# Kernel tuning notes

Measured on AMD Instinct MI355X. Metric: run time of the kernel, lower is better.

## Reference

```python
import jax, jax.numpy as jnp
import numpy as np

B = 4096
N_FEATS = 2048
N_TAGS = 300
RNN_IN = 512
RNN_HID = 512
HID = 512


def setup_inputs() -> dict:
    key = jax.random.key(0)
    ks = jax.random.split(key, 16)
    sc = 0.05  # small weight init, like get_init_weights
    inp = {
        "v": jax.random.normal(ks[0], (B, N_FEATS), jnp.float32),
        "s": jax.random.normal(ks[1], (B, N_TAGS), jnp.float32),
        "decoder_input": jax.random.normal(ks[2], (B, RNN_IN), jnp.float32),
        "rnn_h": jax.random.normal(ks[3], (B, HID), jnp.float32),
        "rnn_c": jax.random.normal(ks[4], (B, HID), jnp.float32),
        # gate axis g=4 stacks (i, f, o, c); per-gate math is independent,
        # identical to the original per-gate weight matrices.
        "Wa": jax.random.normal(ks[5], (4, RNN_IN, RNN_HID), jnp.float32) * sc,
        "Wb": jax.random.normal(ks[6], (4, N_TAGS, RNN_HID), jnp.float32) * sc,
        "Wc": jax.random.normal(ks[7], (4, RNN_HID, HID), jnp.float32) * sc,
        "Ua": jax.random.normal(ks[8], (4, HID, RNN_HID), jnp.float32) * sc,
        "Ub": jax.random.normal(ks[9], (4, N_TAGS, RNN_HID), jnp.float32) * sc,
        "Uc": jax.random.normal(ks[10], (4, RNN_HID, HID), jnp.float32) * sc,
        "Ca": jax.random.normal(ks[11], (4, N_FEATS, RNN_HID), jnp.float32) * sc,
        "Cb": jax.random.normal(ks[12], (4, N_TAGS, RNN_HID), jnp.float32) * sc,
        "Cc": jax.random.normal(ks[13], (4, RNN_HID, HID), jnp.float32) * sc,
        "b": jnp.zeros((4, HID), jnp.float32),
    }
    return inp


def _step(v, s, x, h, c, Wa, Wb, Wc, Ua, Ub, Uc, Ca, Cb, Cc, b):
    # precompute_mats: tag/visual branch projections (gate-stacked)
    t2 = jnp.einsum("bt,gtr->gbr", s, Wb)   # s @ Wb_*
    t3 = jnp.einsum("bf,gfr->gbr", v, Ca)   # v @ Ca_*
    t4 = jnp.einsum("bt,gtr->gbr", s, Cb)   # s @ Cb_*
    # forward: input/hidden branch projections
    t1 = jnp.einsum("bi,gir->gbr", x, Wa)   # x @ Wa_*
    t5 = jnp.einsum("bt,gtr->gbr", s, Ub)   # s @ Ub_*
    t6 = jnp.einsum("bh,ghr->gbr", h, Ua)   # h @ Ua_*
    # bilinear fusion then second-stage projection per gate
    logits = (
        jnp.einsum("gbr,grh->gbh", t1 * t2, Wc)
        + jnp.einsum("gbr,grh->gbh", t3 * t4, Cc)
        + jnp.einsum("gbr,grh->gbh", t5 * t6, Uc)
        + b[:, None, :]
    )
    i = jax.nn.sigmoid(logits[0])
    f = jax.nn.sigmoid(logits[1])
    o = jax.nn.sigmoid(logits[2])
    g = jnp.tanh(logits[3])
    new_c = f * c + i * g
    new_h = o * jnp.tanh(new_c)
    return new_h, new_c


def reference(v, s, decoder_input, rnn_h, rnn_c, Wa, Wb, Wc, Ua, Ub, Uc, Ca, Cb, Cc, b):
    return _step(v, s, decoder_input, rnn_h, rnn_c, Wa, Wb, Wc, Ua, Ub, Uc, Ca, Cb, Cc, b)
```

## Files before the change

### kernel.cpp

```cpp
#include <hip/hip_runtime.h>
#include <hip/hip_bf16.h>
#include <stdint.h>

#define B_DIM 4096
#define NFEATS 2048
#define NTAGS 300
#define NTAGSP 320
#define RIN 512
#define RHID 512
#define HIDD 512
#define KCAT 1536

typedef __attribute__((ext_vector_type(8))) short short8;
typedef __attribute__((ext_vector_type(8))) unsigned short ushort8;
typedef __attribute__((ext_vector_type(4))) float f32x4;

typedef __attribute__((address_space(3))) unsigned int lds_u32_t;
typedef __attribute__((address_space(1))) const unsigned int glb_u32_t;

__device__ __forceinline__ unsigned short f2bf(float f) {
  union { float f; unsigned u; } x; x.f = f;
  unsigned r = (x.u + 0x7fffu + ((x.u >> 16) & 1u)) >> 16;
  return (unsigned short)r;
}
__device__ __forceinline__ float bf2f(unsigned short u) {
  union { unsigned u; float f; } x; x.u = ((unsigned)u) << 16;
  return x.f;
}

__device__ __forceinline__ void gl2lds16(const void* g, void* l) {
  __builtin_amdgcn_global_load_lds((glb_u32_t*)g, (lds_u32_t*)l, 16, 0, 0);
}

__device__ __forceinline__ void sbar() {
  asm volatile("" ::: "memory");
  __builtin_amdgcn_s_barrier();
  asm volatile("" ::: "memory");
}
#define VMCNT4()   asm volatile("s_waitcnt vmcnt(4)" ::: "memory")
#define VMCNT0()   asm volatile("s_waitcnt vmcnt(0)" ::: "memory")
#define LGKMCNT0() asm volatile("s_waitcnt lgkmcnt(0)" ::: "memory")

__global__ void cvt_all(const float* __restrict__ v, const float* __restrict__ x,
                        const float* __restrict__ h, const float* __restrict__ s,
                        unsigned short* __restrict__ vb, unsigned short* __restrict__ xb,
                        unsigned short* __restrict__ hb, unsigned short* __restrict__ sb) {
  int seg = blockIdx.y;
  const float* src; unsigned short* dst; int sc, dc;
  if (seg == 0)      { src = v; dst = vb; sc = NFEATS; dc = NFEATS; }
  else if (seg == 1) { src = x; dst = xb; sc = RIN;    dc = RIN; }
  else if (seg == 2) { src = h; dst = hb; sc = RHID;   dc = RHID; }
  else               { src = s; dst = sb; sc = NTAGS;  dc = NTAGSP; }
  int cpr = dc >> 3;
  long nch = (long)B_DIM * cpr;
  for (long i = (long)blockIdx.x * blockDim.x + threadIdx.x; i < nch;
       i += (long)gridDim.x * blockDim.x) {
    int r = (int)(i / cpr);
    int c0 = (int)(i - (long)r * cpr) << 3;
    const float* sp = src + (long)r * sc + c0;
    ushort8 o;
#pragma unroll
    for (int j = 0; j < 8; ++j) {
      float f = (c0 + j < sc) ? sp[j] : 0.f;
      o[j] = f2bf(f);
    }
    *(ushort8*)(dst + (i << 3)) = o;
  }
}

struct TD { const float* src; unsigned short* dst; int K; int dstLd; int dstOff; int kx0; };
struct TP { TD d[9]; };

__global__ void trans_all(TP tp) {
  __shared__ float t[32][33];
  int bx = blockIdx.x;
  int m = 0;
#pragma unroll
  for (int i = 1; i < 9; ++i)
    if (bx >= tp.d[i].kx0) m = i;
  TD td = tp.d[m];
  int g = blockIdx.z;
  const float* s = td.src + (long)g * td.K * 512;
  unsigned short* d = td.dst + (long)g * 512 * td.dstLd;
  int k0 = (bx - td.kx0) * 32, n0 = blockIdx.y * 32;
  int tx = threadIdx.x, ty = threadIdx.y;
#pragma unroll
  for (int r = 0; r < 4; ++r) {
    int k = k0 + ty + r * 8;
    t[ty + r * 8][tx] = (k < td.K) ? s[(long)k * 512 + n0 + tx] : 0.f;
  }
  __syncthreads();
#pragma unroll
  for (int r = 0; r < 4; ++r) {
    int n = n0 + ty + r * 8;
    d[(long)n * td.dstLd + td.dstOff + k0 + tx] = f2bf(t[tx][ty + r * 8]);
  }
}


__device__ __forceinline__ void stage_half(const unsigned short* mat, int ld,
                                           int gRow0, int k0, char* ldsHalf,
                                           int rl0, int scb, int dstoff) {
  const char* s0 = (const char*)(mat + (long)(gRow0 + rl0) * ld + k0) + scb;
  const char* s1 = (const char*)(mat + (long)(gRow0 + 64 + rl0) * ld + k0) + scb;
  gl2lds16(s0, ldsHalf + dstoff);
  gl2lds16(s1, ldsHalf + 8192 + dstoff);
}

__device__ __forceinline__ void mfma_q(f32x4 (&acc)[8][4], int mb, int nb,
                                       const short8 (&af)[4][2], const short8 (&bf)[2][2]) {
  __builtin_amdgcn_s_setprio(1);
#pragma unroll
  for (int m = 0; m < 4; ++m)
#pragma unroll
    for (int n = 0; n < 2; ++n)
#pragma unroll
      for (int kk = 0; kk < 2; ++kk)
        acc[mb + m][nb + n] =
            __builtin_amdgcn_mfma_f32_16x16x32_bf16(af[m][kk], bf[n][kk], acc[mb + m][nb + n], 0, 0, 0);
  __builtin_amdgcn_s_setprio(0);
}

__device__ __forceinline__ void gemm8_core(const unsigned short* __restrict__ A, int lda,
                                           const unsigned short* __restrict__ Bm, int ldb,
                                           int nt, int rowBase, int colBase,
                                           char* smem, int tid, f32x4 (&acc)[8][4]) {
  char* Ab0 = smem;
  char* Bb0 = smem + 65536;
  int l = tid & 63, w = tid >> 6;
  int wr = w >> 2, wc = w & 3;
  int lr = l & 15, lg = l >> 4;
  int LA = lr * 128 + ((lg * 16) ^ ((lr & 7) << 4));
  int rl0 = tid >> 3;
  int scb = ((tid & 7) << 4) ^ ((rl0 & 7) << 4);
  int dstoff = (tid & ~63) << 4;

#pragma unroll
  for (int mi = 0; mi < 8; ++mi)
#pragma unroll
    for (int ni = 0; ni < 4; ++ni)
#pragma unroll
      for (int r = 0; r < 4; ++r) acc[mi][ni][r] = 0.f;

  stage_half(A, lda, rowBase, 0, Ab0, rl0, scb, dstoff);
  stage_half(A, lda, rowBase + 128, 0, Ab0 + 16384, rl0, scb, dstoff);
  stage_half(Bm, ldb, colBase, 0, Bb0, rl0, scb, dstoff);
  stage_half(Bm, ldb, colBase + 128, 0, Bb0 + 16384, rl0, scb, dstoff);
  if (nt > 1) {
    stage_half(A, lda, rowBase, 64, Ab0 + 32768, rl0, scb, dstoff);
    stage_half(A, lda, rowBase + 128, 64, Ab0 + 49152, rl0, scb, dstoff);
    VMCNT4();
  } else {
    VMCNT0();
  }
  sbar();

  for (int g = 0; g < nt; ++g) {
    int cur = g & 1;
    char* Ab = Ab0 + cur * 32768 + wr * 16384;
    char* Bb = Bb0 + cur * 32768 + wc * 8192;
    char* BbN = Bb0 + (cur ^ 1) * 32768;
    short8 a[4][2], b0[2][2], b1[2][2];

#pragma unroll
    for (int m = 0; m < 4; ++m) {
      a[m][0] = *(const short8*)(Ab + m * 2048 + LA);
      a[m][1] = *(const short8*)(Ab + m * 2048 + (LA ^ 64));
    }
#pragma unroll
    for (int n = 0; n < 2; ++n) {
      b0[n][0] = *(const short8*)(Bb + n * 2048 + LA);
      b0[n][1] = *(const short8*)(Bb + n * 2048 + (LA ^ 64));
    }
    if (g + 1 < nt) stage_half(Bm, ldb, colBase, (g + 1) * 64, BbN, rl0, scb, dstoff);
    sbar();
    LGKMCNT0();
    mfma_q(acc, 0, 0, a, b0);
    sbar();

#pragma unroll
    for (int n = 0; n < 2; ++n) {
      b1[n][0] = *(const short8*)(Bb + 4096 + n * 2048 + LA);
      b1[n][1] = *(const short8*)(Bb + 4096 + n * 2048 + (LA ^ 64));
    }
    if (g + 1 < nt) stage_half(Bm, ldb, colBase + 128, (g + 1) * 64, BbN + 16384, rl0, scb, dstoff);
    sbar();
    LGKMCNT0();
    mfma_q(acc, 0, 2, a, b1);
    sbar();

#pragma unroll
    for (int m = 0; m < 4; ++m) {
      a[m][0] = *(const short8*)(Ab + 8192 + m * 2048 + LA);
      a[m][1] = *(const short8*)(Ab + 8192 + m * 2048 + (LA ^ 64));
    }
    sbar();
    LGKMCNT0();
    mfma_q(acc, 4, 2, a, b1);
    sbar();

    if (g + 2 < nt) {
      stage_half(A, lda, rowBase, (g + 2) * 64, Ab0 + cur * 32768, rl0, scb, dstoff);
      stage_half(A, lda, rowBase + 128, (g + 2) * 64, Ab0 + cur * 32768 + 16384, rl0, scb, dstoff);
    }
    mfma_q(acc, 4, 0, a, b0);
    if (g + 2 < nt) { VMCNT4(); } else if (g + 1 < nt) { VMCNT0(); }
    sbar();
  }
}


__global__ __launch_bounds__(512, 2) void gemm_ts(const unsigned short* __restrict__ sb,
                                                  const unsigned short* __restrict__ SBT,
                                                  unsigned short* __restrict__ TS) {
  extern __shared__ char smem[];
  int tid = threadIdx.x;
  int rowBase = blockIdx.x * 256, colBase = blockIdx.y * 256;
  f32x4 acc[8][4];
  gemm8_core(sb, NTAGSP, SBT, NTAGSP, 5, rowBase, colBase, smem, tid, acc);

  int l = tid & 63, w = tid >> 6, wr = w >> 2, wc = w & 3, lr = l & 15, lg = l >> 4;
  int branch = colBase >> 11;
  unsigned short* TSb = TS + (long)branch * B_DIM * 2048;
#pragma unroll
  for (int mi = 0; mi < 8; ++mi)
#pragma unroll
    for (int ni = 0; ni < 4; ++ni) {
      int colg = (colBase & 2047) + wc * 64 + ni * 16 + lr;
      int row0 = rowBase + wr * 128 + mi * 16 + lg * 4;
#pragma unroll
      for (int r = 0; r < 4; ++r)
        TSb[(long)(row0 + r) * 2048 + colg] = f2bf(acc[mi][ni][r]);
    }
}

__global__ __launch_bounds__(512, 2) void gemm_bil(
    const unsigned short* __restrict__ vb, const unsigned short* __restrict__ xb,
    const unsigned short* __restrict__ hb,
    const unsigned short* __restrict__ CaT, const unsigned short* __restrict__ WaT,
    const unsigned short* __restrict__ UaT,
    const unsigned short* __restrict__ TS, unsigned short* __restrict__ P) {
  extern __shared__ char smem[];
  int tid = threadIdx.x;
  int z = blockIdx.y >> 3;
  int rowBase = blockIdx.x * 256, colBase = (blockIdx.y & 7) * 256;
  const unsigned short *A1, *B1;
  int K1, nt, coff;
  if (z == 0)      { A1 = vb; B1 = CaT; K1 = NFEATS; nt = 32; coff = 512; }
  else if (z == 1) { A1 = xb; B1 = WaT; K1 = RIN;    nt = 8;  coff = 0; }
  else             { A1 = hb; B1 = UaT; K1 = RHID;   nt = 8;  coff = 1024; }

  f32x4 acc[8][4];
  gemm8_core(A1, K1, B1, K1, nt, rowBase, colBase, smem, tid, acc);

  int l = tid & 63, w = tid >> 6, wr = w >> 2, wc = w & 3, lr = l & 15, lg = l >> 4;
  const unsigned short* TSz = TS + (long)z * B_DIM * 2048;
#pragma unroll
  for (int mi = 0; mi < 8; ++mi)
#pragma unroll
    for (int ni = 0; ni < 4; ++ni) {
      int colg = colBase + wc * 64 + ni * 16 + lr;
      int gate = colg >> 9;
      int col = coff + (colg & 511);
      int row0 = rowBase + wr * 128 + mi * 16 + lg * 4;
      unsigned short* Pg = P + (long)gate * B_DIM * KCAT;
#pragma unroll
      for (int r = 0; r < 4; ++r) {
        float ts = bf2f(TSz[(long)(row0 + r) * 2048 + colg]);
        Pg[(long)(row0 + r) * KCAT + col] = f2bf(acc[mi][ni][r] * ts);
      }
    }
}

__global__ __launch_bounds__(512, 2) void gemm_lg(const unsigned short* __restrict__ P,
                                                  const unsigned short* __restrict__ WcT,
                                                  const float* __restrict__ bias,
                                                  float* __restrict__ logits) {
  extern __shared__ char smem[];
  int tid = threadIdx.x;
  int gate = blockIdx.z;
  int rowBase = blockIdx.x * 256, colBase = blockIdx.y * 256;
  const unsigned short* Pg  = P + (long)gate * B_DIM * KCAT;
  const unsigned short* Wg  = WcT + (long)gate * 512 * KCAT;
  f32x4 acc[8][4];
  gemm8_core(Pg, KCAT, Wg, KCAT, 24, rowBase, colBase, smem, tid, acc);

  int l = tid & 63, w = tid >> 6, wr = w >> 2, wc = w & 3, lr = l & 15, lg = l >> 4;
  float* Lg = logits + (long)gate * B_DIM * HIDD;
  const float* bg = bias + gate * HIDD;
#pragma unroll
  for (int mi = 0; mi < 8; ++mi)
#pragma unroll
    for (int ni = 0; ni < 4; ++ni) {
      int col = colBase + wc * 64 + ni * 16 + lr;
      float bv = bg[col];
      int row0 = rowBase + wr * 128 + mi * 16 + lg * 4;
#pragma unroll
      for (int r = 0; r < 4; ++r)
        Lg[(long)(row0 + r) * HIDD + col] = acc[mi][ni][r] + bv;
    }
}

__global__ void lstm_final(const float* __restrict__ logits, const float* __restrict__ c_in,
                           float* __restrict__ out) {
  const long GS = (long)B_DIM * HIDD;
  long i = (long)blockIdx.x * blockDim.x + threadIdx.x;
  if (i >= (GS >> 2)) return;
  f32x4 l0 = *(const f32x4*)(logits + 4 * i);
  f32x4 l1 = *(const f32x4*)(logits + GS + 4 * i);
  f32x4 l2 = *(const f32x4*)(logits + 2 * GS + 4 * i);
  f32x4 l3 = *(const f32x4*)(logits + 3 * GS + 4 * i);
  f32x4 cv = *(const f32x4*)(c_in + 4 * i);
  f32x4 ho, co;
#pragma unroll
  for (int r = 0; r < 4; ++r) {
    float ig = 1.f / (1.f + __expf(-l0[r]));
    float fg = 1.f / (1.f + __expf(-l1[r]));
    float og = 1.f / (1.f + __expf(-l2[r]));
    float gg = tanhf(l3[r]);
    float c = fg * cv[r] + ig * gg;
    co[r] = c;
    ho[r] = og * tanhf(c);
  }
  *(f32x4*)(out + 4 * i) = ho;
  *(f32x4*)(out + GS + 4 * i) = co;
}

extern "C" void kernel_launch(void* const* d_in, const int* in_sizes, int n_in,
                              void* d_out, int out_size, void* d_ws, size_t ws_size,
                              hipStream_t stream) {
  const float* v  = (const float*)d_in[0];
  const float* s  = (const float*)d_in[1];
  const float* x  = (const float*)d_in[2];
  const float* h  = (const float*)d_in[3];
  const float* c  = (const float*)d_in[4];
  const float* Wa = (const float*)d_in[5];
  const float* Wb = (const float*)d_in[6];
  const float* Wc = (const float*)d_in[7];
  const float* Ua = (const float*)d_in[8];
  const float* Ub = (const float*)d_in[9];
  const float* Uc = (const float*)d_in[10];
  const float* Ca = (const float*)d_in[11];
  const float* Cb = (const float*)d_in[12];
  const float* Cc = (const float*)d_in[13];
  const float* bb = (const float*)d_in[14];
  float* out = (float*)d_out;

  char* ws = (char*)d_ws;
  size_t off = 0;
  auto alloc = [&](size_t bytes) {
    char* p = ws + off;
    off = (off + bytes + 255) & ~(size_t)255;
    return p;
  };
  unsigned short* vb    = (unsigned short*)alloc((size_t)B_DIM * NFEATS * 2);
  unsigned short* sb    = (unsigned short*)alloc((size_t)B_DIM * NTAGSP * 2);
  unsigned short* xb    = (unsigned short*)alloc((size_t)B_DIM * RIN * 2);
  unsigned short* hb    = (unsigned short*)alloc((size_t)B_DIM * RHID * 2);
  unsigned short* WaT   = (unsigned short*)alloc((size_t)4 * 512 * 512 * 2);
  unsigned short* UaT   = (unsigned short*)alloc((size_t)4 * 512 * 512 * 2);
  unsigned short* CaT   = (unsigned short*)alloc((size_t)4 * 512 * NFEATS * 2);
  unsigned short* WcatT = (unsigned short*)alloc((size_t)4 * 512 * KCAT * 2);
  unsigned short* SBT   = (unsigned short*)alloc((size_t)3 * 2048 * NTAGSP * 2);
  unsigned short* TSb   = (unsigned short*)alloc((size_t)3 * B_DIM * 2048 * 2);
  unsigned short* Pbuf  = (unsigned short*)alloc((size_t)4 * B_DIM * KCAT * 2);
  float*          Lg    = (float*)TSb;

  cvt_all<<<dim3(512, 4), 256, 0, stream>>>(v, x, h, s, vb, xb, hb, sb);

  TP tp;
  tp.d[0] = { Wa, WaT,                  512, 512,  0,    0   };
  tp.d[1] = { Wb, SBT + 2048 * 320,     300, 320,  0,    16  };
  tp.d[2] = { Ua, UaT,                  512, 512,  0,    26  };
  tp.d[3] = { Ub, SBT + 2 * 2048 * 320, 300, 320,  0,    42  };
  tp.d[4] = { Ca, CaT,                 2048, 2048, 0,    52  };
  tp.d[5] = { Cb, SBT,                  300, 320,  0,    116 };
  tp.d[6] = { Wc, WcatT,                512, 1536, 0,    126 };
  tp.d[7] = { Cc, WcatT,                512, 1536, 512,  142 };
  tp.d[8] = { Uc, WcatT,                512, 1536, 1024, 158 };
  trans_all<<<dim3(174, 16, 4), dim3(32, 8), 0, stream>>>(tp);

  hipFuncSetAttribute((const void*)gemm_ts,  hipFuncAttributeMaxDynamicSharedMemorySize, 131072);
  hipFuncSetAttribute((const void*)gemm_bil, hipFuncAttributeMaxDynamicSharedMemorySize, 131072);
  hipFuncSetAttribute((const void*)gemm_lg,  hipFuncAttributeMaxDynamicSharedMemorySize, 131072);

  gemm_ts<<<dim3(16, 24), 512, 131072, stream>>>(sb, SBT, TSb);
  gemm_bil<<<dim3(16, 24), 512, 131072, stream>>>(vb, xb, hb, CaT, WaT, UaT, TSb, Pbuf);
  gemm_lg<<<dim3(16, 2, 4), 512, 131072, stream>>>(Pbuf, WcatT, bb, Lg);

  lstm_final<<<(B_DIM * HIDD / 4 + 255) / 256, 256, 0, stream>>>(Lg, c, out);
}
```

Before: 197.9 us.

## Use 128-row tiles for heavy GEMMs to balance work across CUs

Templates the GEMM core on the M-tile height so some GEMMs can use 128x256 tiles instead of 256x256. The v@Ca branch of the bilinear GEMM now uses 256 small-tile blocks, while the x/h branches keep big tiles and run in a flattened 1D grid. The output-logit GEMM is also moved to 128-row tiles with less LDS. The goal is more blocks, better CU occupancy and less tail imbalance. The cost is less operand reuse per block and more B-tile reloads.

```diff
diff --git a/kernel.cpp b/kernel.cpp
--- a/kernel.cpp
+++ b/kernel.cpp
@@ -38,6 +38,7 @@
   asm volatile("" ::: "memory");
 }
 #define VMCNT4()   asm volatile("s_waitcnt vmcnt(4)" ::: "memory")
+#define VMCNT2()   asm volatile("s_waitcnt vmcnt(2)" ::: "memory")
 #define VMCNT0()   asm volatile("s_waitcnt vmcnt(0)" ::: "memory")
 #define LGKMCNT0() asm volatile("s_waitcnt lgkmcnt(0)" ::: "memory")
 
@@ -107,11 +108,12 @@
   gl2lds16(s1, ldsHalf + 8192 + dstoff);
 }
 
-__device__ __forceinline__ void mfma_q(f32x4 (&acc)[8][4], int mb, int nb,
-                                       const short8 (&af)[4][2], const short8 (&bf)[2][2]) {
+template<int MFR>
+__device__ __forceinline__ void mfma_q(f32x4 (&acc)[2 * MFR][4], int mb, int nb,
+                                       const short8 (&af)[MFR][2], const short8 (&bf)[2][2]) {
   __builtin_amdgcn_s_setprio(1);
 #pragma unroll
-  for (int m = 0; m < 4; ++m)
+  for (int m = 0; m < MFR; ++m)
 #pragma unroll
     for (int n = 0; n < 2; ++n)
 #pragma unroll
@@ -121,12 +123,14 @@
   __builtin_amdgcn_s_setprio(0);
 }
 
+template<int MFR>
 __device__ __forceinline__ void gemm8_core(const unsigned short* __restrict__ A, int lda,
                                            const unsigned short* __restrict__ Bm, int ldb,
                                            int nt, int rowBase, int colBase,
-                                           char* smem, int tid, f32x4 (&acc)[8][4]) {
+                                           char* smem, int tid, f32x4 (&acc)[2 * MFR][4]) {
+  constexpr int ATILE = 8192 * MFR;
   char* Ab0 = smem;
-  char* Bb0 = smem + 65536;
+  char* Bb0 = smem + 2 * ATILE;
   int l = tid & 63, w = tid >> 6;
   int wr = w >> 2, wc = w & 3;
   int lr = l & 15, lg = l >> 4;
@@ -136,20 +140,20 @@
   int dstoff = (tid & ~63) << 4;
 
 #pragma unroll
-  for (int mi = 0; mi < 8; ++mi)
+  for (int mi = 0; mi < 2 * MFR; ++mi)
 #pragma unroll
     for (int ni = 0; ni < 4; ++ni)
 #pragma unroll
       for (int r = 0; r < 4; ++r) acc[mi][ni][r] = 0.f;
 
   stage_half(A, lda, rowBase, 0, Ab0, rl0, scb, dstoff);
-  stage_half(A, lda, rowBase + 128, 0, Ab0 + 16384, rl0, scb, dstoff);
+  if constexpr (MFR == 4) stage_half(A, lda, rowBase + 128, 0, Ab0 + ATILE / 2, rl0, scb, dstoff);
   stage_half(Bm, ldb, colBase, 0, Bb0, rl0, scb, dstoff);
   stage_half(Bm, ldb, colBase + 128, 0, Bb0 + 16384, rl0, scb, dstoff);
   if (nt > 1) {
-    stage_half(A, lda, rowBase, 64, Ab0 + 32768, rl0, scb, dstoff);
-    stage_half(A, lda, rowBase + 128, 64, Ab0 + 49152, rl0, scb, dstoff);
-    VMCNT4();
+    stage_half(A, lda, rowBase, 64, Ab0 + ATILE, rl0, scb, dstoff);
+    if constexpr (MFR == 4) stage_half(A, lda, rowBase + 128, 64, Ab0 + ATILE + ATILE / 2, rl0, scb, dstoff);
+    if constexpr (MFR == 4) { VMCNT4(); } else { VMCNT2(); }
   } else {
     VMCNT0();
   }
@@ -157,13 +161,13 @@
 
   for (int g = 0; g < nt; ++g) {
     int cur = g & 1;
-    char* Ab = Ab0 + cur * 32768 + wr * 16384;
+    char* Ab = Ab0 + cur * ATILE + wr * (ATILE / 2);
     char* Bb = Bb0 + cur * 32768 + wc * 8192;
     char* BbN = Bb0 + (cur ^ 1) * 32768;
-    short8 a[4][2], b0[2][2], b1[2][2];
-
-#pragma unroll
-    for (int m = 0; m < 4; ++m) {
+    short8 a[MFR][2], b0[2][2], b1[2][2];
+
+#pragma unroll
+    for (int m = 0; m < MFR; ++m) {
       a[m][0] = *(const short8*)(Ab + m * 2048 + LA);
       a[m][1] = *(const short8*)(Ab + m * 2048 + (LA ^ 64));
     }
@@ -175,7 +179,7 @@
     if (g + 1 < nt) stage_half(Bm, ldb, colBase, (g + 1) * 64, BbN, rl0, scb, dstoff);
     sbar();
     LGKMCNT0();
-    mfma_q(acc, 0, 0, a, b0);
+    mfma_q<MFR>(acc, 0, 0, a, b0);
     sbar();
 
 #pragma unroll
@@ -186,25 +190,30 @@
     if (g + 1 < nt) stage_half(Bm, ldb, colBase + 128, (g + 1) * 64, BbN + 16384, rl0, scb, dstoff);
     sbar();
     LGKMCNT0();
-    mfma_q(acc, 0, 2, a, b1);
-    sbar();
-
-#pragma unroll
-    for (int m = 0; m < 4; ++m) {
-      a[m][0] = *(const short8*)(Ab + 8192 + m * 2048 + LA);
-      a[m][1] = *(const short8*)(Ab + 8192 + m * 2048 + (LA ^ 64));
+    mfma_q<MFR>(acc, 0, 2, a, b1);
+    sbar();
+
+#pragma unroll
+    for (int m = 0; m < MFR; ++m) {
+      a[m][0] = *(const short8*)(Ab + ATILE / 4 + m * 2048 + LA);
+      a[m][1] = *(const short8*)(Ab + ATILE / 4 + m * 2048 + (LA ^ 64));
     }
     sbar();
     LGKMCNT0();
-    mfma_q(acc, 4, 2, a, b1);
+    mfma_q<MFR>(acc, MFR, 2, a, b1);
     sbar();
 
     if (g + 2 < nt) {
-      stage_half(A, lda, rowBase, (g + 2) * 64, Ab0 + cur * 32768, rl0, scb, dstoff);
-      stage_half(A, lda, rowBase + 128, (g + 2) * 64, Ab0 + cur * 32768 + 16384, rl0, scb, dstoff);
-    }
-    mfma_q(acc, 4, 0, a, b0);
-    if (g + 2 < nt) { VMCNT4(); } else if (g + 1 < nt) { VMCNT0(); }
+      stage_half(A, lda, rowBase, (g + 2) * 64, Ab0 + cur * ATILE, rl0, scb, dstoff);
+      if constexpr (MFR == 4)
+        stage_half(A, lda, rowBase + 128, (g + 2) * 64, Ab0 + cur * ATILE + ATILE / 2, rl0, scb, dstoff);
+    }
+    mfma_q<MFR>(acc, MFR, 0, a, b0);
+    if (g + 2 < nt) {
+      if constexpr (MFR == 4) { VMCNT4(); } else { VMCNT2(); }
+    } else if (g + 1 < nt) {
+      VMCNT0();
+    }
     sbar();
   }
 }
@@ -217,7 +226,7 @@
   int tid = threadIdx.x;
   int rowBase = blockIdx.x * 256, colBase = blockIdx.y * 256;
   f32x4 acc[8][4];
-  gemm8_core(sb, NTAGSP, SBT, NTAGSP, 5, rowBase, colBase, smem, tid, acc);
+  gemm8_core<4>(sb, NTAGSP, SBT, NTAGSP, 5, rowBase, colBase, smem, tid, acc);
 
   int l = tid & 63, w = tid >> 6, wr = w >> 2, wc = w & 3, lr = l & 15, lg = l >> 4;
   int branch = colBase >> 11;
@@ -242,34 +251,57 @@
     const unsigned short* __restrict__ TS, unsigned short* __restrict__ P) {
   extern __shared__ char smem[];
   int tid = threadIdx.x;
-  int z = blockIdx.y >> 3;
-  int rowBase = blockIdx.x * 256, colBase = (blockIdx.y & 7) * 256;
-  const unsigned short *A1, *B1;
-  int K1, nt, coff;
-  if (z == 0)      { A1 = vb; B1 = CaT; K1 = NFEATS; nt = 32; coff = 512; }
-  else if (z == 1) { A1 = xb; B1 = WaT; K1 = RIN;    nt = 8;  coff = 0; }
-  else             { A1 = hb; B1 = UaT; K1 = RHID;   nt = 8;  coff = 1024; }
-
-  f32x4 acc[8][4];
-  gemm8_core(A1, K1, B1, K1, nt, rowBase, colBase, smem, tid, acc);
-
+  int bid = blockIdx.x;
   int l = tid & 63, w = tid >> 6, wr = w >> 2, wc = w & 3, lr = l & 15, lg = l >> 4;
-  const unsigned short* TSz = TS + (long)z * B_DIM * 2048;
-#pragma unroll
-  for (int mi = 0; mi < 8; ++mi)
-#pragma unroll
-    for (int ni = 0; ni < 4; ++ni) {
-      int colg = colBase + wc * 64 + ni * 16 + lr;
-      int gate = colg >> 9;
-      int col = coff + (colg & 511);
-      int row0 = rowBase + wr * 128 + mi * 16 + lg * 4;
-      unsigned short* Pg = P + (long)gate * B_DIM * KCAT;
-#pragma unroll
-      for (int r = 0; r < 4; ++r) {
-        float ts = bf2f(TSz[(long)(row0 + r) * 2048 + colg]);
-        Pg[(long)(row0 + r) * KCAT + col] = f2bf(acc[mi][ni][r] * ts);
+
+  if (bid < 256) {
+    int rowBase = (bid & 31) * 128, colBase = (bid >> 5) * 256;
+    f32x4 acc[4][4];
+    gemm8_core<2>(vb, NFEATS, CaT, NFEATS, NFEATS / 64, rowBase, colBase, smem, tid, acc);
+
+    const unsigned short* TSz = TS;
+#pragma unroll
+    for (int mi = 0; mi < 4; ++mi)
+#pragma unroll
+      for (int ni = 0; ni < 4; ++ni) {
+        int colg = colBase + wc * 64 + ni * 16 + lr;
+        int gate = colg >> 9;
+        int col = 512 + (colg & 511);
+        int row0 = rowBase + wr * 64 + mi * 16 + lg * 4;
+        unsigned short* Pg = P + (long)gate * B_DIM * KCAT;
+#pragma unroll
+        for (int r = 0; r < 4; ++r) {
+          float ts = bf2f(TSz[(long)(row0 + r) * 2048 + colg]);
+          Pg[(long)(row0 + r) * KCAT + col] = f2bf(acc[mi][ni][r] * ts);
+        }
       }
-    }
+  } else {
+    int t = bid - 256;
+    int z = 1 + (t >> 7); t &= 127;
+    int rowBase = (t & 15) * 256, colBase = (t >> 4) * 256;
+    const unsigned short* A1 = (z == 1) ? xb : hb;
+    const unsigned short* B1 = (z == 1) ? WaT : UaT;
+    int coff = (z == 1) ? 0 : 1024;
+    f32x4 acc[8][4];
+    gemm8_core<4>(A1, RIN, B1, RIN, RIN / 64, rowBase, colBase, smem, tid, acc);
+
+    const unsigned short* TSz = TS + (long)z * B_DIM * 2048;
+#pragma unroll
+    for (int mi = 0; mi < 8; ++mi)
+#pragma unroll
+      for (int ni = 0; ni < 4; ++ni) {
+        int colg = colBase + wc * 64 + ni * 16 + lr;
+        int gate = colg >> 9;
+        int col = coff + (colg & 511);
+        int row0 = rowBase + wr * 128 + mi * 16 + lg * 4;
+        unsigned short* Pg = P + (long)gate * B_DIM * KCAT;
+#pragma unroll
+        for (int r = 0; r < 4; ++r) {
+          float ts = bf2f(TSz[(long)(row0 + r) * 2048 + colg]);
+          Pg[(long)(row0 + r) * KCAT + col] = f2bf(acc[mi][ni][r] * ts);
+        }
+      }
+  }
 }
 
 __global__ __launch_bounds__(512, 2) void gemm_lg(const unsigned short* __restrict__ P,
@@ -279,22 +311,22 @@
   extern __shared__ char smem[];
   int tid = threadIdx.x;
   int gate = blockIdx.z;
-  int rowBase = blockIdx.x * 256, colBase = blockIdx.y * 256;
-  const unsigned short* Pg  = P + (long)gate * B_DIM * KCAT;
-  const unsigned short* Wg  = WcT + (long)gate * 512 * KCAT;
-  f32x4 acc[8][4];
-  gemm8_core(Pg, KCAT, Wg, KCAT, 24, rowBase, colBase, smem, tid, acc);
+  int rowBase = blockIdx.x * 128, colBase = blockIdx.y * 256;
+  const unsigned short* Pg = P + (long)gate * B_DIM * KCAT;
+  const unsigned short* Wg = WcT + (long)gate * 512 * KCAT;
+  f32x4 acc[4][4];
+  gemm8_core<2>(Pg, KCAT, Wg, KCAT, KCAT / 64, rowBase, colBase, smem, tid, acc);
 
   int l = tid & 63, w = tid >> 6, wr = w >> 2, wc = w & 3, lr = l & 15, lg = l >> 4;
   float* Lg = logits + (long)gate * B_DIM * HIDD;
   const float* bg = bias + gate * HIDD;
 #pragma unroll
-  for (int mi = 0; mi < 8; ++mi)
+  for (int mi = 0; mi < 4; ++mi)
 #pragma unroll
     for (int ni = 0; ni < 4; ++ni) {
       int col = colBase + wc * 64 + ni * 16 + lr;
       float bv = bg[col];
-      int row0 = rowBase + wr * 128 + mi * 16 + lg * 4;
+      int row0 = rowBase + wr * 64 + mi * 16 + lg * 4;
 #pragma unroll
       for (int r = 0; r < 4; ++r)
         Lg[(long)(row0 + r) * HIDD + col] = acc[mi][ni][r] + bv;
@@ -382,11 +414,11 @@
 
   hipFuncSetAttribute((const void*)gemm_ts,  hipFuncAttributeMaxDynamicSharedMemorySize, 131072);
   hipFuncSetAttribute((const void*)gemm_bil, hipFuncAttributeMaxDynamicSharedMemorySize, 131072);
-  hipFuncSetAttribute((const void*)gemm_lg,  hipFuncAttributeMaxDynamicSharedMemorySize, 131072);
+  hipFuncSetAttribute((const void*)gemm_lg,  hipFuncAttributeMaxDynamicSharedMemorySize, 98304);
 
   gemm_ts<<<dim3(16, 24), 512, 131072, stream>>>(sb, SBT, TSb);
-  gemm_bil<<<dim3(16, 24), 512, 131072, stream>>>(vb, xb, hb, CaT, WaT, UaT, TSb, Pbuf);
-  gemm_lg<<<dim3(16, 2, 4), 512, 131072, stream>>>(Pbuf, WcatT, bb, Lg);
+  gemm_bil<<<dim3(512), 512, 131072, stream>>>(vb, xb, hb, CaT, WaT, UaT, TSb, Pbuf);
+  gemm_lg<<<dim3(32, 2, 4), 512, 98304, stream>>>(Pbuf, WcatT, bb, Lg);
 
   lstm_final<<<(B_DIM * HIDD / 4 + 255) / 256, 256, 0, stream>>>(Lg, c, out);
 }
```

Result: faster. 186.7 us (-5.6%).
